# Kernel optimization log

Measured on AMD Instinct MI355X. Metric: run time of the kernel, lower is better.

The kernel has to match this reference:

```python
import jax, jax.numpy as jnp
import numpy as np

B, S, D, H = 64, 2048, 512, 512


def setup_inputs() -> dict:
    key = jax.random.key(0)
    ks = jax.random.split(key, 8)
    scale_in = 1.0 / np.sqrt(D)
    scale_v = 1.0 / np.sqrt(H)
    return {
        "x": jax.random.normal(ks[0], (B, D), jnp.float32),
        "context": jax.random.normal(ks[1], (B, S, D), jnp.float32),
        "mask": jax.random.randint(ks[2], (B, S), 0, 2).astype(bool),
        "W_in": jax.random.normal(ks[3], (H, D), jnp.float32) * scale_in,
        "b_in": jax.random.normal(ks[4], (H,), jnp.float32) * scale_in,
        "W_ctx": jax.random.normal(ks[5], (H, D), jnp.float32) * scale_in,
        "b_ctx": jax.random.normal(ks[6], (H,), jnp.float32) * scale_in,
        "V": jax.random.uniform(ks[7], (H,), jnp.float32, -scale_v, scale_v),
    }


def reference(x, context, mask, W_in, b_in, W_ctx, b_ctx, V):
    # inp: Linear(input) -> [B, H], broadcast over S
    inp = x @ W_in.T + b_in  # [B, H]
    # ctx: 1x1 Conv1d over permuted context == per-position linear -> [B, H, S]
    ctx = jnp.einsum("bsd,hd->bhs", context, W_ctx) + b_ctx[None, :, None]
    # additive (Bahdanau) scores: V . tanh(inp + ctx) -> [B, S]
    att = jnp.einsum("h,bhs->bs", V, jnp.tanh(inp[:, :, None] + ctx))
    # mask selected positions with -inf, softmax over seq dim
    att = jnp.where(mask, -jnp.inf, att)
    alpha = jax.nn.softmax(att, axis=1)  # [B, S]
    # weighted sum of ctx columns -> [B, H]
    hidden_state = jnp.einsum("bhs,bs->bh", ctx, alpha)
    return hidden_state, alpha
```

## Files before the change

kernel.cpp:

```cpp
#include <hip/hip_runtime.h>
#include <hip/hip_bf16.h>
#include <cstdint>

#define B_ 64
#define S_ 2048
#define D_ 512
#define H_ 512

typedef short s16x8 __attribute__((ext_vector_type(8)));
typedef float f32x4 __attribute__((ext_vector_type(4)));

static __device__ __forceinline__ unsigned short f2bf(float f) {
  __bf16 h = (__bf16)f;
  return __builtin_bit_cast(unsigned short, h);
}

__global__ __launch_bounds__(256) void k_prep(
    const unsigned int* __restrict__ mw, int* __restrict__ flags,
    const float* __restrict__ W, unsigned short* __restrict__ Wp,
    const float* __restrict__ x, const float* __restrict__ W_in,
    const float* __restrict__ b_in, const float* __restrict__ b_ctx,
    float* __restrict__ inp_pb) {
  const int bx = blockIdx.x;
  const int t = threadIdx.x;
  if (bx < 128) {
    __shared__ int blk;
    if (t == 0) blk = 0;
    __syncthreads();
    unsigned w = mw[bx * 256 + t];
    int bits = 0;
    if (w == 0x3F800000u) bits = 2;
    else if (w > 1u) bits = 1;
    unsigned long long a1 = __ballot(bits & 1);
    unsigned long long a2 = __ballot(bits & 2);
    if ((t & 63) == 0) {
      int v = (a1 ? 1 : 0) | (a2 ? 2 : 0);
      if (v) atomicOr(&blk, v);
    }
    __syncthreads();
    if (t == 0) flags[bx] = blk;
  } else if (bx < 256) {
    const int tid = (bx - 128) * 256 + t;
    const int lane = tid & 63;
    const int hb = (tid >> 6) & 31;
    const int kb = tid >> 11;
    const int h = hb * 16 + (lane & 15);
    const int k = kb * 32 + (lane >> 4) * 8;
    const float* src = W + (size_t)h * D_ + k;
    float4 a = *(const float4*)src;
    float4 c = *(const float4*)(src + 4);
    s16x8 o;
    o[0] = (short)f2bf(a.x); o[1] = (short)f2bf(a.y);
    o[2] = (short)f2bf(a.z); o[3] = (short)f2bf(a.w);
    o[4] = (short)f2bf(c.x); o[5] = (short)f2bf(c.y);
    o[6] = (short)f2bf(c.z); o[7] = (short)f2bf(c.w);
    *(s16x8*)(Wp + (size_t)tid * 8) = o;
  } else {
    const int bb = bx - 256;
    const int b = bb >> 2, hq = bb & 3;
    __shared__ float xs[D_];
    xs[t] = x[b * D_ + t];
    xs[t + 256] = x[b * D_ + t + 256];
    __syncthreads();
    const int h = hq * 128 + (t >> 1);
    const int half = t & 1;
    const float4* wr = (const float4*)(W_in + (size_t)h * D_) + half * 64;
    const float* xh = xs + half * 256;
    float acc = 0.f;
#pragma unroll 4
    for (int d4 = 0; d4 < 64; ++d4) {
      float4 w = wr[d4];
      acc += w.x * xh[d4 * 4] + w.y * xh[d4 * 4 + 1] + w.z * xh[d4 * 4 + 2] +
             w.w * xh[d4 * 4 + 3];
    }
    acc += __shfl_xor(acc, 1, 64);
    if (half == 0) inp_pb[b * H_ + h] = acc + b_in[h] + b_ctx[h];
  }
}

__global__ __launch_bounds__(512, 2) void k_att(
    const float* __restrict__ context, const unsigned short* __restrict__ Wp,
    const float* __restrict__ inp_pb, const float* __restrict__ V,
    float* __restrict__ att) {
  __shared__ char bt[2][8192];
  __shared__ float red[8][64];
  const int tid = threadIdx.x;
  const int wave = tid >> 6, lane = tid & 63;
  const int b = blockIdx.y, s0 = blockIdx.x * 64;
  const float* ctxb = context + ((size_t)b * S_ + s0) * D_;
  const int hbase = wave * 64;
  const int bln = lane & 15, blh = lane >> 4;

  const int srow = tid >> 3, kc8 = (tid & 7) * 8;
  const int sbyte = srow * 128 + ((kc8 * 2) ^ ((srow & 7) << 4));
  const float* gsrc = ctxb + (size_t)srow * D_ + kc8;

  const unsigned short* ap = Wp + ((size_t)(wave * 4) * 64 + lane) * 8;

  f32x4 acc[4][4];
#pragma unroll
  for (int m = 0; m < 4; ++m)
#pragma unroll
    for (int n = 0; n < 4; ++n) acc[m][n] = f32x4{0.f, 0.f, 0.f, 0.f};

  f32x4 sg0a, sg0b, sg1a, sg1b, sg2a, sg2b;
#define LOAD_SET0(T) { sg0a = __builtin_nontemporal_load((const f32x4*)(gsrc + (T)*64)); \
                       sg0b = __builtin_nontemporal_load((const f32x4*)(gsrc + (T)*64 + 4)); }
#define LOAD_SET1(T) { sg1a = __builtin_nontemporal_load((const f32x4*)(gsrc + (T)*64)); \
                       sg1b = __builtin_nontemporal_load((const f32x4*)(gsrc + (T)*64 + 4)); }
#define LOAD_SET2(T) { sg2a = __builtin_nontemporal_load((const f32x4*)(gsrc + (T)*64)); \
                       sg2b = __builtin_nontemporal_load((const f32x4*)(gsrc + (T)*64 + 4)); }
#define CVT_SET(A, Bv, BUF) { s16x8 hb_; \
    hb_[0] = (short)f2bf((A)[0]); hb_[1] = (short)f2bf((A)[1]); \
    hb_[2] = (short)f2bf((A)[2]); hb_[3] = (short)f2bf((A)[3]); \
    hb_[4] = (short)f2bf((Bv)[0]); hb_[5] = (short)f2bf((Bv)[1]); \
    hb_[6] = (short)f2bf((Bv)[2]); hb_[7] = (short)f2bf((Bv)[3]); \
    *(s16x8*)(&bt[BUF][sbyte]) = hb_; }

  LOAD_SET0(0);
  LOAD_SET1(1);
  LOAD_SET2(2);
  CVT_SET(sg0a, sg0b, 0);
  asm volatile("s_waitcnt lgkmcnt(0)" ::: "memory");
  __builtin_amdgcn_s_barrier();
  __builtin_amdgcn_sched_barrier(0);

#pragma unroll
  for (int t = 0; t < 8; ++t) {
    const char* cur = bt[t & 1];
    s16x8 bfrag[2][4];
#pragma unroll
    for (int kk = 0; kk < 2; ++kk)
#pragma unroll
      for (int n = 0; n < 4; ++n) {
        const int sr = n * 16 + bln;
        const int off = (kk * 64 + blh * 16) ^ ((sr & 7) << 4);
        bfrag[kk][n] = *(const s16x8*)(cur + sr * 128 + off);
      }
    s16x8 af[2][4];
#pragma unroll
    for (int kk = 0; kk < 2; ++kk)
#pragma unroll
      for (int m = 0; m < 4; ++m)
        af[kk][m] = *(const s16x8*)(ap + (size_t)(t * 2 + kk) * 32 * 512 +
                                    (size_t)m * 512);
    if (t < 5) {
      const int s3 = (t + 3) % 3;
      if (s3 == 0) LOAD_SET0(t + 3)
      else if (s3 == 1) LOAD_SET1(t + 3)
      else LOAD_SET2(t + 3)
    }
    __builtin_amdgcn_s_setprio(1);
#pragma unroll
    for (int kk = 0; kk < 2; ++kk)
#pragma unroll
      for (int m = 0; m < 4; ++m)
#pragma unroll
        for (int n = 0; n < 4; ++n)
          acc[m][n] = __builtin_amdgcn_mfma_f32_16x16x32_bf16(af[kk][m],
                                                              bfrag[kk][n],
                                                              acc[m][n], 0, 0, 0);
    __builtin_amdgcn_s_setprio(0);
    if (t < 7) {
      const int s1 = (t + 1) % 3;
      const int nb = (t + 1) & 1;
      if (s1 == 0) CVT_SET(sg0a, sg0b, nb)
      else if (s1 == 1) CVT_SET(sg1a, sg1b, nb)
      else CVT_SET(sg2a, sg2b, nb)
    }
    asm volatile("s_waitcnt lgkmcnt(0)" ::: "memory");
    __builtin_amdgcn_s_barrier();
    __builtin_amdgcn_sched_barrier(0);
  }
#undef LOAD_SET0
#undef LOAD_SET1
#undef LOAD_SET2
#undef CVT_SET

  float attp[4] = {0.f, 0.f, 0.f, 0.f};
  const float* ib = inp_pb + b * H_;
#pragma unroll
  for (int m = 0; m < 4; ++m) {
#pragma unroll
    for (int j = 0; j < 4; ++j) {
      int h = hbase + m * 16 + (blh << 2) + j;
      float c = ib[h];
      float vh = V[h];
#pragma unroll
      for (int n = 0; n < 4; ++n) {
        float x = acc[m][n][j] + c;
        float e = __expf(2.f * x);
        float tt = 1.f - 2.f * __builtin_amdgcn_rcpf(e + 1.f);
        attp[n] += vh * tt;
      }
    }
  }
#pragma unroll
  for (int n = 0; n < 4; ++n) {
    attp[n] += __shfl_xor(attp[n], 16, 64);
    attp[n] += __shfl_xor(attp[n], 32, 64);
  }
  if (lane < 16) {
#pragma unroll
    for (int n = 0; n < 4; ++n) red[wave][n * 16 + lane] = attp[n];
  }
  __syncthreads();
  if (tid < 64) {
    float s = 0.f;
#pragma unroll
    for (int w = 0; w < 8; ++w) s += red[w][tid];
    att[(size_t)b * S_ + s0 + tid] = s;
  }
}

__global__ void k_softmax(const float* __restrict__ att, const void* __restrict__ mask,
                          const int* __restrict__ flags, float* __restrict__ alpha) {
  const int b = blockIdx.x, t = threadIdx.x;
  __shared__ int cshared;
  __shared__ float sm[4];
  if (t < 64) {
    int v = flags[t] | flags[t + 64];
    for (int off = 32; off; off >>= 1) v |= __shfl_xor(v, off, 64);
    if (t == 0) cshared = v;
  }
  __syncthreads();
  const int c = cshared;
  const int mtype = (c & 2) ? 2 : (c & 1);
  const unsigned char* m8 = (const unsigned char*)mask;
  const int* m32 = (const int*)mask;
  const float* mf = (const float*)mask;
  float vals[8];
  float mx = -3.0e38f;
#pragma unroll
  for (int i = 0; i < 8; ++i) {
    int s = t + i * 256;
    size_t idx = (size_t)b * S_ + s;
    int msk = (mtype == 1) ? (int)m8[idx] : (mtype == 2) ? (mf[idx] != 0.f) : m32[idx];
    float v = msk ? -__builtin_inff() : att[idx];
    vals[i] = v;
    mx = fmaxf(mx, v);
  }
  for (int off = 32; off; off >>= 1) mx = fmaxf(mx, __shfl_xor(mx, off, 64));
  if ((t & 63) == 0) sm[t >> 6] = mx;
  __syncthreads();
  mx = fmaxf(fmaxf(sm[0], sm[1]), fmaxf(sm[2], sm[3]));
  float es[8];
  float sum = 0.f;
#pragma unroll
  for (int i = 0; i < 8; ++i) {
    es[i] = __expf(vals[i] - mx);
    sum += es[i];
  }
  for (int off = 32; off; off >>= 1) sum += __shfl_xor(sum, off, 64);
  __syncthreads();
  if ((t & 63) == 0) sm[t >> 6] = sum;
  __syncthreads();
  sum = sm[0] + sm[1] + sm[2] + sm[3];
  float inv = __fdividef(1.f, sum);
#pragma unroll
  for (int i = 0; i < 8; ++i) alpha[(size_t)b * S_ + t + i * 256] = es[i] * inv;
}

__global__ void k_ypart(const float* __restrict__ context,
                        const float* __restrict__ alpha, float* __restrict__ y_part) {
  const int chunk = 7 - blockIdx.x, b = 63 - blockIdx.y, t = threadIdx.x;
  __shared__ float al[256];
  __shared__ float4 part[128];
  al[t] = alpha[(size_t)b * S_ + chunk * 256 + t];
  __syncthreads();
  const int d4 = t & 127, sr = t >> 7;
  const float4* base = (const float4*)(context + ((size_t)b * S_ + chunk * 256) * D_);
  float4 acc = make_float4(0.f, 0.f, 0.f, 0.f);
  for (int i = 0; i < 128; ++i) {
    int s = sr + 2 * i;
    float4 v = base[(size_t)s * 128 + d4];
    float a = al[s];
    acc.x += a * v.x; acc.y += a * v.y; acc.z += a * v.z; acc.w += a * v.w;
  }
  if (sr == 1) part[d4] = acc;
  __syncthreads();
  if (sr == 0) {
    float4 o = part[d4];
    o.x += acc.x; o.y += acc.y; o.z += acc.z; o.w += acc.w;
    *(float4*)(y_part + ((size_t)(b * 8 + chunk)) * D_ + d4 * 4) = o;
  }
}

__global__ __launch_bounds__(256) void k_hidden(
    const float* __restrict__ y_part, const float* __restrict__ W_ctx,
    const float* __restrict__ b_ctx, float* __restrict__ hidden) {
  const int bx = blockIdx.x;
  const int b = bx >> 2, hq = bx & 3;
  const int t = threadIdx.x;
  __shared__ float ys[D_];
  for (int d = t; d < D_; d += 256) {
    float s = 0.f;
#pragma unroll
    for (int c = 0; c < 8; ++c) s += y_part[((size_t)(b * 8 + c)) * D_ + d];
    ys[d] = s;
  }
  __syncthreads();
  const int h = hq * 128 + (t >> 1);
  const int half = t & 1;
  const float4* wr = (const float4*)(W_ctx + (size_t)h * D_) + half * 64;
  const float* yh = ys + half * 256;
  float acc = 0.f;
#pragma unroll 4
  for (int d4 = 0; d4 < 64; ++d4) {
    float4 w = wr[d4];
    acc += w.x * yh[d4 * 4] + w.y * yh[d4 * 4 + 1] + w.z * yh[d4 * 4 + 2] +
           w.w * yh[d4 * 4 + 3];
  }
  acc += __shfl_xor(acc, 1, 64);
  if (half == 0) hidden[b * H_ + h] = acc + b_ctx[h];
}

extern "C" void kernel_launch(void* const* d_in, const int* in_sizes, int n_in,
                              void* d_out, int out_size, void* d_ws, size_t ws_size,
                              hipStream_t stream) {
  (void)in_sizes; (void)n_in; (void)out_size; (void)ws_size;
  const float* x = (const float*)d_in[0];
  const float* context = (const float*)d_in[1];
  const void* mask = d_in[2];
  const float* W_in = (const float*)d_in[3];
  const float* b_in = (const float*)d_in[4];
  const float* W_ctx = (const float*)d_in[5];
  const float* b_ctx = (const float*)d_in[6];
  const float* V = (const float*)d_in[7];

  float* out_hidden = (float*)d_out;
  float* out_alpha = (float*)d_out + B_ * H_;

  char* ws = (char*)d_ws;
  float* inp_pb = (float*)ws;
  float* att = (float*)(ws + 131072);
  float* y_part = (float*)(ws + 655360);
  int* flags = (int*)(ws + 1703936);
  unsigned short* Wp = (unsigned short*)(ws + 1704448);

  k_prep<<<512, 256, 0, stream>>>((const unsigned int*)mask, flags, W_ctx, Wp,
                                  x, W_in, b_in, b_ctx, inp_pb);
  k_att<<<dim3(S_ / 64, B_), 512, 0, stream>>>(context, Wp, inp_pb, V, att);
  k_softmax<<<B_, 256, 0, stream>>>(att, mask, flags, out_alpha);
  k_ypart<<<dim3(8, B_), 256, 0, stream>>>(context, out_alpha, y_part);
  k_hidden<<<256, 256, 0, stream>>>(y_part, W_ctx, b_ctx, out_hidden);
}
```

Baseline: 182.5 us.

## Fuse softmax into attention kernel and hidden projection into ypart via last-block counters

Removes two kernel launches by folding the per-batch softmax into k_att and the W_ctx projection into k_ypart. In each case the last-finishing block for a batch row, found with a threadfence plus an atomic counter, does the follow-up work. The counters are reset in k_prep. This saves launch gaps and the tail of small kernels. In exchange, the softmax and the 512x512 matvec now run serially inside a single block per batch, with one thread per output row, which can lengthen the tail.

```diff
diff --git a/kernel.cpp b/kernel.cpp
--- a/kernel.cpp
+++ b/kernel.cpp
@@ -17,6 +17,7 @@
 
 __global__ __launch_bounds__(256) void k_prep(
     const unsigned int* __restrict__ mw, int* __restrict__ flags,
+    int* __restrict__ done, int* __restrict__ done2,
     const float* __restrict__ W, unsigned short* __restrict__ Wp,
     const float* __restrict__ x, const float* __restrict__ W_in,
     const float* __restrict__ b_in, const float* __restrict__ b_ctx,
@@ -26,6 +27,10 @@
   if (bx < 128) {
     __shared__ int blk;
     if (t == 0) blk = 0;
+    if (t == 128) {
+      if (bx < 64) done[bx] = 0;
+      else done2[bx - 64] = 0;
+    }
     __syncthreads();
     unsigned w = mw[bx * 256 + t];
     int bits = 0;
@@ -81,7 +86,9 @@
 __global__ __launch_bounds__(512, 2) void k_att(
     const float* __restrict__ context, const unsigned short* __restrict__ Wp,
     const float* __restrict__ inp_pb, const float* __restrict__ V,
-    float* __restrict__ att) {
+    float* __restrict__ att, const void* __restrict__ mask,
+    const int* __restrict__ flags, int* __restrict__ done,
+    float* __restrict__ alpha) {
   __shared__ char bt[2][8192];
   __shared__ float red[8][64];
   const int tid = threadIdx.x;
@@ -211,17 +218,24 @@
     for (int w = 0; w < 8; ++w) s += red[w][tid];
     att[(size_t)b * S_ + s0 + tid] = s;
   }
-}
-
-__global__ void k_softmax(const float* __restrict__ att, const void* __restrict__ mask,
-                          const int* __restrict__ flags, float* __restrict__ alpha) {
-  const int b = blockIdx.x, t = threadIdx.x;
+
+  __shared__ int lastflag;
   __shared__ int cshared;
-  __shared__ float sm[4];
-  if (t < 64) {
-    int v = flags[t] | flags[t + 64];
+  __shared__ float sm[8];
+  __syncthreads();
+  if (tid == 0) {
+    __threadfence();
+    int old = atomicAdd(&done[b], 1);
+    lastflag = (old == 31);
+  }
+  __syncthreads();
+  if (!lastflag) return;
+  __threadfence();
+
+  if (tid < 64) {
+    int v = flags[tid] | flags[tid + 64];
     for (int off = 32; off; off >>= 1) v |= __shfl_xor(v, off, 64);
-    if (t == 0) cshared = v;
+    if (tid == 0) cshared = v;
   }
   __syncthreads();
   const int c = cshared;
@@ -229,11 +243,11 @@
   const unsigned char* m8 = (const unsigned char*)mask;
   const int* m32 = (const int*)mask;
   const float* mf = (const float*)mask;
-  float vals[8];
+  float vals[4];
   float mx = -3.0e38f;
 #pragma unroll
-  for (int i = 0; i < 8; ++i) {
-    int s = t + i * 256;
+  for (int i = 0; i < 4; ++i) {
+    int s = tid + i * 512;
     size_t idx = (size_t)b * S_ + s;
     int msk = (mtype == 1) ? (int)m8[idx] : (mtype == 2) ? (mf[idx] != 0.f) : m32[idx];
     float v = msk ? -__builtin_inff() : att[idx];
@@ -241,28 +255,36 @@
     mx = fmaxf(mx, v);
   }
   for (int off = 32; off; off >>= 1) mx = fmaxf(mx, __shfl_xor(mx, off, 64));
-  if ((t & 63) == 0) sm[t >> 6] = mx;
-  __syncthreads();
-  mx = fmaxf(fmaxf(sm[0], sm[1]), fmaxf(sm[2], sm[3]));
-  float es[8];
+  if (lane == 0) sm[wave] = mx;
+  __syncthreads();
+  mx = sm[0];
+#pragma unroll
+  for (int w = 1; w < 8; ++w) mx = fmaxf(mx, sm[w]);
+  float es[4];
   float sum = 0.f;
 #pragma unroll
-  for (int i = 0; i < 8; ++i) {
+  for (int i = 0; i < 4; ++i) {
     es[i] = __expf(vals[i] - mx);
     sum += es[i];
   }
   for (int off = 32; off; off >>= 1) sum += __shfl_xor(sum, off, 64);
   __syncthreads();
-  if ((t & 63) == 0) sm[t >> 6] = sum;
-  __syncthreads();
-  sum = sm[0] + sm[1] + sm[2] + sm[3];
+  if (lane == 0) sm[wave] = sum;
+  __syncthreads();
+  sum = 0.f;
+#pragma unroll
+  for (int w = 0; w < 8; ++w) sum += sm[w];
   float inv = __fdividef(1.f, sum);
 #pragma unroll
-  for (int i = 0; i < 8; ++i) alpha[(size_t)b * S_ + t + i * 256] = es[i] * inv;
-}
-
-__global__ void k_ypart(const float* __restrict__ context,
-                        const float* __restrict__ alpha, float* __restrict__ y_part) {
+  for (int i = 0; i < 4; ++i)
+    alpha[(size_t)b * S_ + tid + i * 512] = es[i] * inv;
+}
+
+__global__ __launch_bounds__(256) void k_ypart(
+    const float* __restrict__ context, const float* __restrict__ alpha,
+    float* __restrict__ y_part, const float* __restrict__ W_ctx,
+    const float* __restrict__ b_ctx, float* __restrict__ hidden,
+    int* __restrict__ done2) {
   const int chunk = 7 - blockIdx.x, b = 63 - blockIdx.y, t = threadIdx.x;
   __shared__ float al[256];
   __shared__ float4 part[128];
@@ -284,35 +306,37 @@
     o.x += acc.x; o.y += acc.y; o.z += acc.z; o.w += acc.w;
     *(float4*)(y_part + ((size_t)(b * 8 + chunk)) * D_ + d4 * 4) = o;
   }
-}
-
-__global__ __launch_bounds__(256) void k_hidden(
-    const float* __restrict__ y_part, const float* __restrict__ W_ctx,
-    const float* __restrict__ b_ctx, float* __restrict__ hidden) {
-  const int bx = blockIdx.x;
-  const int b = bx >> 2, hq = bx & 3;
-  const int t = threadIdx.x;
+
+  __shared__ int lastflag;
+  __syncthreads();
+  if (t == 0) {
+    __threadfence();
+    int old = atomicAdd(&done2[b], 1);
+    lastflag = (old == 7);
+  }
+  __syncthreads();
+  if (!lastflag) return;
+  __threadfence();
+
   __shared__ float ys[D_];
   for (int d = t; d < D_; d += 256) {
     float s = 0.f;
 #pragma unroll
-    for (int c = 0; c < 8; ++c) s += y_part[((size_t)(b * 8 + c)) * D_ + d];
+    for (int c2 = 0; c2 < 8; ++c2) s += y_part[((size_t)(b * 8 + c2)) * D_ + d];
     ys[d] = s;
   }
   __syncthreads();
-  const int h = hq * 128 + (t >> 1);
-  const int half = t & 1;
-  const float4* wr = (const float4*)(W_ctx + (size_t)h * D_) + half * 64;
-  const float* yh = ys + half * 256;
-  float acc = 0.f;
+  for (int h = t; h < H_; h += 256) {
+    const float4* wr = (const float4*)(W_ctx + (size_t)h * D_);
+    float acc2 = 0.f;
 #pragma unroll 4
-  for (int d4 = 0; d4 < 64; ++d4) {
-    float4 w = wr[d4];
-    acc += w.x * yh[d4 * 4] + w.y * yh[d4 * 4 + 1] + w.z * yh[d4 * 4 + 2] +
-           w.w * yh[d4 * 4 + 3];
-  }
-  acc += __shfl_xor(acc, 1, 64);
-  if (half == 0) hidden[b * H_ + h] = acc + b_ctx[h];
+    for (int d4b = 0; d4b < 128; ++d4b) {
+      float4 w = wr[d4b];
+      acc2 += w.x * ys[d4b * 4] + w.y * ys[d4b * 4 + 1] + w.z * ys[d4b * 4 + 2] +
+              w.w * ys[d4b * 4 + 3];
+    }
+    hidden[b * H_ + h] = acc2 + b_ctx[h];
+  }
 }
 
 extern "C" void kernel_launch(void* const* d_in, const int* in_sizes, int n_in,
@@ -336,12 +360,14 @@
   float* att = (float*)(ws + 131072);
   float* y_part = (float*)(ws + 655360);
   int* flags = (int*)(ws + 1703936);
-  unsigned short* Wp = (unsigned short*)(ws + 1704448);
-
-  k_prep<<<512, 256, 0, stream>>>((const unsigned int*)mask, flags, W_ctx, Wp,
-                                  x, W_in, b_in, b_ctx, inp_pb);
-  k_att<<<dim3(S_ / 64, B_), 512, 0, stream>>>(context, Wp, inp_pb, V, att);
-  k_softmax<<<B_, 256, 0, stream>>>(att, mask, flags, out_alpha);
-  k_ypart<<<dim3(8, B_), 256, 0, stream>>>(context, out_alpha, y_part);
-  k_hidden<<<256, 256, 0, stream>>>(y_part, W_ctx, b_ctx, out_hidden);
-}
+  int* done = (int*)(ws + 1704448);
+  int* done2 = (int*)(ws + 1704704);
+  unsigned short* Wp = (unsigned short*)(ws + 1704960);
+
+  k_prep<<<512, 256, 0, stream>>>((const unsigned int*)mask, flags, done, done2,
+                                  W_ctx, Wp, x, W_in, b_in, b_ctx, inp_pb);
+  k_att<<<dim3(S_ / 64, B_), 512, 0, stream>>>(context, Wp, inp_pb, V, att,
+                                               mask, flags, done, out_alpha);
+  k_ypart<<<dim3(8, B_), 256, 0, stream>>>(context, out_alpha, y_part, W_ctx,
+                                           b_ctx, out_hidden, done2);
+}
```

Measured after the change: 437.7 us. 140% more time.
